# Optimization experiments

Measured on AMD Instinct MI355X. Metric: run time of the kernel, lower is better.

## Reference

```python
import jax, jax.numpy as jnp
import numpy as np

D_MODEL = 1024
N_HEADS = 16
HEAD_DIM = D_MODEL // N_HEADS
BATCH = 2
SEQ = 2048


def setup_inputs() -> dict:
    key = jax.random.key(0)
    ks = jax.random.split(key, 9)
    s = 1.0 / np.sqrt(D_MODEL)
    inp = {
        "x": jax.random.normal(ks[0], (BATCH, SEQ, D_MODEL), dtype=jnp.float32),
        "Wq": jax.random.uniform(ks[1], (D_MODEL, D_MODEL), jnp.float32, -s, s),
        "bq": jax.random.uniform(ks[2], (D_MODEL,), jnp.float32, -s, s),
        "Wk": jax.random.uniform(ks[3], (D_MODEL, D_MODEL), jnp.float32, -s, s),
        "bk": jax.random.uniform(ks[4], (D_MODEL,), jnp.float32, -s, s),
        "Wv": jax.random.uniform(ks[5], (D_MODEL, D_MODEL), jnp.float32, -s, s),
        "bv": jax.random.uniform(ks[6], (D_MODEL,), jnp.float32, -s, s),
        "Wo": jax.random.uniform(ks[7], (D_MODEL, D_MODEL), jnp.float32, -s, s),
        "bo": jax.random.uniform(ks[8], (D_MODEL,), jnp.float32, -s, s),
    }
    return inp


def reference(x, Wq, bq, Wk, bk, Wv, bv, Wo, bo):
    B, S, _ = x.shape
    # projections -> [B, H, S, Dh]
    def proj(W, b):
        y = jnp.einsum('bsd,df->bsf', x, W) + b
        return y.reshape(B, S, N_HEADS, HEAD_DIM).transpose(0, 2, 1, 3)
    q = proj(Wq, bq)
    k = proj(Wk, bk)
    v = proj(Wv, bv)
    scores = jnp.einsum('bhqd,bhkd->bhqk', q, k) / jnp.sqrt(jnp.float32(HEAD_DIM))
    mask = jnp.tril(jnp.ones((S, S), dtype=bool))  # [S, S] causal mask
    scores = jnp.where(mask, scores, -jnp.inf)
    weights = jax.nn.softmax(scores, axis=-1)
    h = jnp.einsum('bhqk,bhkd->bhqd', weights, v)
    h = h.transpose(0, 2, 1, 3).reshape(B, S, N_HEADS * HEAD_DIM)
    return jnp.einsum('bsd,df->bsf', h, Wo) + bo
```

## Files before the change

kernel.cpp:

```cpp
#include <hip/hip_runtime.h>
#include <hip/hip_bf16.h>
#include <cmath>

#define D_MODEL 1024
#define NHEADS 16
#define HDIM 64
#define BATCH 2
#define SEQ 2048
#define MROWS (BATCH*SEQ)
#define KDIM 1024

typedef unsigned short ushort_t;
typedef unsigned int uint32;
typedef __attribute__((ext_vector_type(8))) short short8;
typedef __attribute__((ext_vector_type(4))) float floatx4;

#define QSCALE 0.1803368801111204f
#define EXP2F(x) __builtin_amdgcn_exp2f(x)

__device__ __forceinline__ ushort_t f2bf(float x) {
    union { float f; uint32 u; } v; v.f = x;
    uint32 r = v.u + 0x7FFFu + ((v.u >> 16) & 1u);
    return (ushort_t)(r >> 16);
}

__device__ __forceinline__ uint32 pkbf(float a, float b) {
    union { __hip_bfloat162 h2; uint32 u; } v;
    v.h2 = __float22bfloat162_rn(make_float2(a, b));
    return v.u;
}

__device__ __forceinline__ void glds16(const void* g, void* l) {
    __builtin_amdgcn_global_load_lds(
        (const __attribute__((address_space(1))) void*)g,
        (__attribute__((address_space(3))) void*)l, 16, 0, 0);
}

__global__ __launch_bounds__(256)
void cvt_all(const float* __restrict__ x, const float* __restrict__ W0,
             const float* __restrict__ W1, const float* __restrict__ W2,
             const float* __restrict__ W3, ushort_t* __restrict__ xb,
             ushort_t* __restrict__ WtQKV, ushort_t* __restrict__ WtO)
{
    const int z = blockIdx.z;
    if (z == 4) {
        size_t idx = ((size_t)blockIdx.y * 32 + blockIdx.x) * 256 + threadIdx.x;
        #pragma unroll
        for (int l = 0; l < 4; ++l) {
            size_t i = ((size_t)l * 262144 + idx) * 4;
            float4 v = *(const float4*)(x + i);
            uint2 o;
            o.x = pkbf(v.x, v.y);
            o.y = pkbf(v.z, v.w);
            *(uint2*)(xb + i) = o;
        }
        return;
    }
    __shared__ float tl[32][33];
    const float* W = (z == 0) ? W0 : (z == 1) ? W1 : (z == 2) ? W2 : W3;
    ushort_t* out = (z < 3) ? (WtQKV + (size_t)z * D_MODEL * KDIM) : WtO;
    const int k0 = blockIdx.x * 32, n0 = blockIdx.y * 32;
    const int tx = threadIdx.x & 31, ty = threadIdx.x >> 5;
    #pragma unroll
    for (int i = 0; i < 4; ++i)
        tl[ty + i * 8][tx] = W[(size_t)(k0 + ty + i * 8) * D_MODEL + n0 + tx];
    __syncthreads();
    #pragma unroll
    for (int i = 0; i < 4; ++i)
        out[(size_t)(n0 + ty + i * 8) * KDIM + k0 + tx] = f2bf(tl[tx][ty + i * 8]);
}

__global__ __launch_bounds__(128, 2)
void gemm_qkv(const ushort_t* __restrict__ A, const ushort_t* __restrict__ Bt,
              const float* __restrict__ b0, const float* __restrict__ b1,
              const float* __restrict__ b2, ushort_t* __restrict__ Qb,
              ushort_t* __restrict__ Kb, ushort_t* __restrict__ Vb)
{
    __shared__ ushort_t As[128 * 64];
    __shared__ ushort_t Bs[128 * 64];

    const int tid = threadIdx.x;
    const int w = tid >> 6, lane = tid & 63;
    const int quad = lane >> 4, col = lane & 15;
    const int m0 = blockIdx.y * 128, n0 = blockIdx.x * 128;

    floatx4 zero = {0.f, 0.f, 0.f, 0.f};
    floatx4 acc[4][8];
    #pragma unroll
    for (int i = 0; i < 4; ++i)
        #pragma unroll
        for (int j = 0; j < 8; ++j) acc[i][j] = zero;

    #pragma unroll 1
    for (int k0 = 0; k0 < KDIM; k0 += 64) {
        #pragma unroll
        for (int i = 0; i < 8; ++i) {
            int c = i * 128 + tid;
            int row = c >> 3;
            int kc = (c & 7) ^ (row & 7);
            glds16(A  + (size_t)(m0 + row) * KDIM + k0 + kc * 8, As + (i * 128 + w * 64) * 8);
            glds16(Bt + (size_t)(n0 + row) * KDIM + k0 + kc * 8, Bs + (i * 128 + w * 64) * 8);
        }
        __syncthreads();
        #pragma unroll
        for (int ks = 0; ks < 2; ++ks) {
            short8 af[4], bfr[8];
            const int kc = ks * 4 + quad;
            #pragma unroll
            for (int mt = 0; mt < 4; ++mt) {
                int r = w * 64 + mt * 16 + col;
                af[mt] = *(const short8*)(As + ((size_t)r * 8 + (kc ^ (r & 7))) * 8);
            }
            #pragma unroll
            for (int nt = 0; nt < 8; ++nt) {
                int r = nt * 16 + col;
                bfr[nt] = *(const short8*)(Bs + ((size_t)r * 8 + (kc ^ (r & 7))) * 8);
            }
            #pragma unroll
            for (int mt = 0; mt < 4; ++mt)
                #pragma unroll
                for (int nt = 0; nt < 8; ++nt)
                    acc[mt][nt] = __builtin_amdgcn_mfma_f32_16x16x32_bf16(
                        af[mt], bfr[nt], acc[mt][nt], 0, 0, 0);
        }
        __syncthreads();
    }

    const int which = n0 >> 10;
    const float* bp = (which == 0) ? b0 : (which == 1) ? b1 : b2;
    if (which < 2) {
        ushort_t* outp = (which == 0) ? Qb : Kb;
        const float scl = (which == 0) ? QSCALE : 1.0f;
        #pragma unroll
        for (int mt = 0; mt < 4; ++mt)
            #pragma unroll
            for (int nt = 0; nt < 8; ++nt) {
                int nn = (n0 + nt * 16 + col) & 1023;
                float bb = bp[nn];
                int h = nn >> 6, d = nn & 63;
                #pragma unroll
                for (int r = 0; r < 4; ++r) {
                    int m = m0 + w * 64 + mt * 16 + quad * 4 + r;
                    int b = m >> 11, s = m & 2047;
                    outp[((size_t)(b * NHEADS + h) * SEQ + s) * HDIM + d] =
                        f2bf((acc[mt][nt][r] + bb) * scl);
                }
            }
    } else {
        #pragma unroll
        for (int mt = 0; mt < 4; ++mt)
            #pragma unroll
            for (int nt = 0; nt < 8; ++nt) {
                int nn = (n0 + nt * 16 + col) & 1023;
                float bb = bp[nn];
                int h = nn >> 6, d = nn & 63;
                int mb = m0 + w * 64 + mt * 16 + quad * 4;
                int b = mb >> 11, s = mb & 2047;
                uint2 pw;
                pw.x = pkbf(acc[mt][nt][0] + bb, acc[mt][nt][1] + bb);
                pw.y = pkbf(acc[mt][nt][2] + bb, acc[mt][nt][3] + bb);
                *(uint2*)(Vb + ((size_t)(b * NHEADS + h) * HDIM + d) * SEQ + s) = pw;
            }
    }
}

__global__ __launch_bounds__(128, 2)
void gemm_o(const ushort_t* __restrict__ A, const ushort_t* __restrict__ Bt,
            const float* __restrict__ b0, float* __restrict__ Cf)
{
    __shared__ ushort_t As[128 * 64];
    __shared__ ushort_t Bs[64 * 64];

    const int tid = threadIdx.x;
    const int w = tid >> 6, lane = tid & 63;
    const int quad = lane >> 4, col = lane & 15;
    const int m0 = blockIdx.y * 128, n0 = blockIdx.x * 64;

    floatx4 zero = {0.f, 0.f, 0.f, 0.f};
    floatx4 acc[4][4];
    #pragma unroll
    for (int i = 0; i < 4; ++i)
        #pragma unroll
        for (int j = 0; j < 4; ++j) acc[i][j] = zero;

    #pragma unroll 1
    for (int k0 = 0; k0 < KDIM; k0 += 64) {
        #pragma unroll
        for (int i = 0; i < 8; ++i) {
            int c = i * 128 + tid;
            int row = c >> 3;
            int kc = (c & 7) ^ (row & 7);
            glds16(A + (size_t)(m0 + row) * KDIM + k0 + kc * 8, As + (i * 128 + w * 64) * 8);
        }
        #pragma unroll
        for (int i = 0; i < 4; ++i) {
            int c = i * 128 + tid;
            int row = c >> 3;
            int kc = (c & 7) ^ (row & 7);
            glds16(Bt + (size_t)(n0 + row) * KDIM + k0 + kc * 8, Bs + (i * 128 + w * 64) * 8);
        }
        __syncthreads();
        #pragma unroll
        for (int ks = 0; ks < 2; ++ks) {
            short8 af[4], bfr[4];
            const int kc = ks * 4 + quad;
            #pragma unroll
            for (int mt = 0; mt < 4; ++mt) {
                int r = w * 64 + mt * 16 + col;
                af[mt] = *(const short8*)(As + ((size_t)r * 8 + (kc ^ (r & 7))) * 8);
            }
            #pragma unroll
            for (int nt = 0; nt < 4; ++nt) {
                int r = nt * 16 + col;
                bfr[nt] = *(const short8*)(Bs + ((size_t)r * 8 + (kc ^ (r & 7))) * 8);
            }
            #pragma unroll
            for (int mt = 0; mt < 4; ++mt)
                #pragma unroll
                for (int nt = 0; nt < 4; ++nt)
                    acc[mt][nt] = __builtin_amdgcn_mfma_f32_16x16x32_bf16(
                        af[mt], bfr[nt], acc[mt][nt], 0, 0, 0);
        }
        __syncthreads();
    }

    #pragma unroll
    for (int mt = 0; mt < 4; ++mt)
        #pragma unroll
        for (int nt = 0; nt < 4; ++nt) {
            int n = n0 + nt * 16 + col;
            float bb = b0[n];
            #pragma unroll
            for (int r = 0; r < 4; ++r) {
                int m = m0 + w * 64 + mt * 16 + quad * 4 + r;
                Cf[(size_t)m * D_MODEL + n] = acc[mt][nt][r] + bb;
            }
        }
}

__global__ __launch_bounds__(256)
void attn_mfma(const ushort_t* __restrict__ Q, const ushort_t* __restrict__ K,
               const ushort_t* __restrict__ Vt, ushort_t* __restrict__ H)
{
    __shared__ ushort_t Qs[64 * 64];
    __shared__ ushort_t Ks[2][64 * 64];
    __shared__ ushort_t Vs[2][64 * 64];
    ushort_t* Ps = Qs;

    const int tid = threadIdx.x;
    const int w = tid >> 6, lane = tid & 63;
    const int quad = lane >> 4, col = lane & 15;
    const int blk = blockIdx.x;
    const int bh = (blk & 7) * 4 + ((blk >> 3) & 3);
    const int pair = blk >> 5;
    const size_t base = (size_t)bh * SEQ * HDIM;
    const ushort_t* Kb = K + base;
    const ushort_t* Vb = Vt + base;
    const int b = bh >> 4, h = bh & 15;

    const int c0 = (w * 2 + 0) * 64 + lane;
    const int c1 = (w * 2 + 1) * 64 + lane;
    const int r0 = c0 >> 3, o0 = ((c0 & 7) ^ (r0 & 7)) * 8;
    const int r1 = c1 >> 3, o1 = ((c1 & 7) ^ (r1 & 7)) * 8;

    const int qloc = w * 16 + col;
    const int rq = qloc;
    const floatx4 zero = {0.f, 0.f, 0.f, 0.f};

    #pragma unroll 1
    for (int pi = 0; pi < 2; ++pi) {
        const int qt = pi ? pair : 31 - pair;
        const int q0 = qt * 64;
        const int nt = qt + 1;

        __syncthreads();
        #pragma unroll
        for (int i = 0; i < 2; ++i) {
            int c = (w * 2 + i) * 64 + lane;
            int row = c >> 3, kc = (c & 7) ^ (row & 7);
            glds16(Q + base + (size_t)(q0 + row) * HDIM + kc * 8, Qs + (w * 2 + i) * 512);
        }
        glds16(Kb + (size_t)r0 * HDIM + o0, Ks[0] + (w * 2 + 0) * 512);
        glds16(Kb + (size_t)r1 * HDIM + o1, Ks[0] + (w * 2 + 1) * 512);
        glds16(Vb + (size_t)r0 * SEQ + o0,  Vs[0] + (w * 2 + 0) * 512);
        glds16(Vb + (size_t)r1 * SEQ + o1,  Vs[0] + (w * 2 + 1) * 512);
        __syncthreads();

        short8 bq[2];
        #pragma unroll
        for (int ks = 0; ks < 2; ++ks) {
            int kc = ks * 4 + quad;
            bq[ks] = *(const short8*)(Qs + ((size_t)rq * 8 + (kc ^ (rq & 7))) * 8);
        }

        floatx4 o[4];
        #pragma unroll
        for (int j = 0; j < 4; ++j) o[j] = zero;
        float lreg = 0.f;

        #pragma unroll 1
        for (int t = 0; t < nt; ++t) {
            const ushort_t* Kcur = Ks[t & 1];
            const ushort_t* Vcur = Vs[t & 1];
            if (t + 1 < nt) {
                const int k0n = (t + 1) * 64;
                ushort_t* Kn = Ks[(t + 1) & 1];
                ushort_t* Vn = Vs[(t + 1) & 1];
                glds16(Kb + (size_t)(k0n + r0) * HDIM + o0, Kn + (w * 2 + 0) * 512);
                glds16(Kb + (size_t)(k0n + r1) * HDIM + o1, Kn + (w * 2 + 1) * 512);
                glds16(Vb + (size_t)r0 * SEQ + k0n + o0,    Vn + (w * 2 + 0) * 512);
                glds16(Vb + (size_t)r1 * SEQ + k0n + o1,    Vn + (w * 2 + 1) * 512);
            }

            floatx4 sc[4];
            #pragma unroll
            for (int j = 0; j < 4; ++j) sc[j] = zero;
            #pragma unroll
            for (int ks = 0; ks < 2; ++ks) {
                const int kc = ks * 4 + quad;
                #pragma unroll
                for (int j = 0; j < 4; ++j) {
                    int rk = j * 16 + col;
                    short8 ak = *(const short8*)(Kcur + ((size_t)rk * 8 + (kc ^ (rk & 7))) * 8);
                    sc[j] = __builtin_amdgcn_mfma_f32_16x16x32_bf16(ak, bq[ks], sc[j], 0, 0, 0);
                }
            }

            if (t == nt - 1) {
                #pragma unroll
                for (int j = 0; j < 4; ++j)
                    #pragma unroll
                    for (int r = 0; r < 4; ++r)
                        if (j * 16 + quad * 4 + r > qloc) sc[j][r] = -INFINITY;
            }

            float ls = 0.f;
            #pragma unroll
            for (int j = 0; j < 4; ++j) {
                float p0 = EXP2F(sc[j][0]);
                float p1 = EXP2F(sc[j][1]);
                float p2 = EXP2F(sc[j][2]);
                float p3 = EXP2F(sc[j][3]);
                ls += (p0 + p1) + (p2 + p3);
                uint2 pw;
                pw.x = pkbf(p0, p1);
                pw.y = pkbf(p2, p3);
                int c = 2 * j + (quad >> 1);
                *(uint2*)(Ps + ((size_t)rq * 8 + (c ^ (rq & 7))) * 8 + (quad & 1) * 4) = pw;
            }
            lreg += ls;

            #pragma unroll
            for (int ks = 0; ks < 2; ++ks) {
                const int kc = ks * 4 + quad;
                short8 bp = *(const short8*)(Ps + ((size_t)rq * 8 + (kc ^ (rq & 7))) * 8);
                #pragma unroll
                for (int j = 0; j < 4; ++j) {
                    int rv = j * 16 + col;
                    short8 av = *(const short8*)(Vcur + ((size_t)rv * 8 + (kc ^ (rv & 7))) * 8);
                    o[j] = __builtin_amdgcn_mfma_f32_16x16x32_bf16(av, bp, o[j], 0, 0, 0);
                }
            }

            __syncthreads();
        }

        lreg += __shfl_xor(lreg, 16);
        lreg += __shfl_xor(lreg, 32);

        const float linv = 1.f / lreg;
        const size_t rowb = ((size_t)(b * SEQ + q0 + qloc)) * D_MODEL + h * HDIM;
        #pragma unroll
        for (int j = 0; j < 4; ++j) {
            uint2 pw;
            pw.x = pkbf(o[j][0] * linv, o[j][1] * linv);
            pw.y = pkbf(o[j][2] * linv, o[j][3] * linv);
            *(uint2*)(H + rowb + j * 16 + quad * 4) = pw;
        }
    }
}

extern "C" void kernel_launch(void* const* d_in, const int* in_sizes, int n_in,
                              void* d_out, int out_size, void* d_ws, size_t ws_size,
                              hipStream_t stream)
{
    (void)in_sizes; (void)n_in; (void)out_size; (void)ws_size;
    const float* x  = (const float*)d_in[0];
    const float* Wq = (const float*)d_in[1];
    const float* bq = (const float*)d_in[2];
    const float* Wk = (const float*)d_in[3];
    const float* bk = (const float*)d_in[4];
    const float* Wv = (const float*)d_in[5];
    const float* bv = (const float*)d_in[6];
    const float* Wo = (const float*)d_in[7];
    const float* bo = (const float*)d_in[8];

    const size_t E = (size_t)MROWS * D_MODEL;
    ushort_t* xb    = (ushort_t*)d_ws;
    ushort_t* WtQKV = xb + E;
    ushort_t* WtO   = WtQKV + 3 * (size_t)D_MODEL * KDIM;
    ushort_t* Qb    = WtO + (size_t)D_MODEL * KDIM;
    ushort_t* Kb    = Qb + E;
    ushort_t* Vb    = Kb + E;
    ushort_t* Hb    = Vb + E;

    cvt_all<<<dim3(32, 32, 5), 256, 0, stream>>>(x, Wq, Wk, Wv, Wo, xb, WtQKV, WtO);
    gemm_qkv<<<dim3(24, 32), 128, 0, stream>>>(xb, WtQKV, bq, bk, bv, Qb, Kb, Vb);
    attn_mfma<<<dim3(512), 256, 0, stream>>>(Qb, Kb, Vb, Hb);
    gemm_o<<<dim3(16, 32), 128, 0, stream>>>(Hb, WtO, bo, (float*)d_out);
}
```

Before: 179.0 us.

## Split attention key tile across waves and reduce partial outputs in shared memory

Each wave now owns 16 keys of the 64-key tile and computes scores for all 64 queries, instead of owning 16 queries against all keys. This removes the P round-trip through shared memory, since P stays in registers and feeds 16x16x16 MFMAs directly. Partial O and row sums are reduced across the four waves through a 66KB shared buffer at the end. In exchange it uses more accumulator registers (64 floats for O), more LDS (which may lower occupancy), and adds a cross-wave reduction on each query tile.

```diff
diff --git a/kernel.cpp b/kernel.cpp
--- a/kernel.cpp
+++ b/kernel.cpp
@@ -13,6 +13,7 @@
 typedef unsigned short ushort_t;
 typedef unsigned int uint32;
 typedef __attribute__((ext_vector_type(8))) short short8;
+typedef __attribute__((ext_vector_type(4))) short short4b;
 typedef __attribute__((ext_vector_type(4))) float floatx4;
 
 #define QSCALE 0.1803368801111204f
@@ -242,10 +243,12 @@
 void attn_mfma(const ushort_t* __restrict__ Q, const ushort_t* __restrict__ K,
                const ushort_t* __restrict__ Vt, ushort_t* __restrict__ H)
 {
-    __shared__ ushort_t Qs[64 * 64];
-    __shared__ ushort_t Ks[2][64 * 64];
-    __shared__ ushort_t Vs[2][64 * 64];
-    ushort_t* Ps = Qs;
+    __shared__ __align__(16) float smemf[16640];
+    ushort_t* Qs  = (ushort_t*)smemf;
+    ushort_t* Ksm = (ushort_t*)(smemf + 2048);
+    ushort_t* Vsm = (ushort_t*)(smemf + 6144);
+    float* Ored = smemf;
+    float* Lred = smemf + 16384;
 
     const int tid = threadIdx.x;
     const int w = tid >> 6, lane = tid & 63;
@@ -263,8 +266,7 @@
     const int r0 = c0 >> 3, o0 = ((c0 & 7) ^ (r0 & 7)) * 8;
     const int r1 = c1 >> 3, o1 = ((c1 & 7) ^ (r1 & 7)) * 8;
 
-    const int qloc = w * 16 + col;
-    const int rq = qloc;
+    const int rk = w * 16 + col;
     const floatx4 zero = {0.f, 0.f, 0.f, 0.f};
 
     #pragma unroll 1
@@ -280,32 +282,37 @@
             int row = c >> 3, kc = (c & 7) ^ (row & 7);
             glds16(Q + base + (size_t)(q0 + row) * HDIM + kc * 8, Qs + (w * 2 + i) * 512);
         }
-        glds16(Kb + (size_t)r0 * HDIM + o0, Ks[0] + (w * 2 + 0) * 512);
-        glds16(Kb + (size_t)r1 * HDIM + o1, Ks[0] + (w * 2 + 1) * 512);
-        glds16(Vb + (size_t)r0 * SEQ + o0,  Vs[0] + (w * 2 + 0) * 512);
-        glds16(Vb + (size_t)r1 * SEQ + o1,  Vs[0] + (w * 2 + 1) * 512);
-        __syncthreads();
-
-        short8 bq[2];
-        #pragma unroll
-        for (int ks = 0; ks < 2; ++ks) {
-            int kc = ks * 4 + quad;
-            bq[ks] = *(const short8*)(Qs + ((size_t)rq * 8 + (kc ^ (rq & 7))) * 8);
-        }
-
-        floatx4 o[4];
-        #pragma unroll
-        for (int j = 0; j < 4; ++j) o[j] = zero;
-        float lreg = 0.f;
+        glds16(Kb + (size_t)r0 * HDIM + o0, Ksm + (w * 2 + 0) * 512);
+        glds16(Kb + (size_t)r1 * HDIM + o1, Ksm + (w * 2 + 1) * 512);
+        glds16(Vb + (size_t)r0 * SEQ + o0,  Vsm + (w * 2 + 0) * 512);
+        glds16(Vb + (size_t)r1 * SEQ + o1,  Vsm + (w * 2 + 1) * 512);
+        __syncthreads();
+
+        short8 bq[4][2];
+        #pragma unroll
+        for (int qb = 0; qb < 4; ++qb)
+            #pragma unroll
+            for (int ks = 0; ks < 2; ++ks) {
+                int rq = qb * 16 + col;
+                int kc = ks * 4 + quad;
+                bq[qb][ks] = *(const short8*)(Qs + ((size_t)rq * 8 + (kc ^ (rq & 7))) * 8);
+            }
+
+        floatx4 o_[4][4];
+        #pragma unroll
+        for (int i = 0; i < 4; ++i)
+            #pragma unroll
+            for (int j = 0; j < 4; ++j) o_[i][j] = zero;
+        float lq[4] = {0.f, 0.f, 0.f, 0.f};
 
         #pragma unroll 1
         for (int t = 0; t < nt; ++t) {
-            const ushort_t* Kcur = Ks[t & 1];
-            const ushort_t* Vcur = Vs[t & 1];
+            const ushort_t* Kcur = Ksm + (t & 1) * 4096;
+            const ushort_t* Vcur = Vsm + (t & 1) * 4096;
             if (t + 1 < nt) {
                 const int k0n = (t + 1) * 64;
-                ushort_t* Kn = Ks[(t + 1) & 1];
-                ushort_t* Vn = Vs[(t + 1) & 1];
+                ushort_t* Kn = Ksm + ((t + 1) & 1) * 4096;
+                ushort_t* Vn = Vsm + ((t + 1) & 1) * 4096;
                 glds16(Kb + (size_t)(k0n + r0) * HDIM + o0, Kn + (w * 2 + 0) * 512);
                 glds16(Kb + (size_t)(k0n + r1) * HDIM + o1, Kn + (w * 2 + 1) * 512);
                 glds16(Vb + (size_t)r0 * SEQ + k0n + o0,    Vn + (w * 2 + 0) * 512);
@@ -314,68 +321,104 @@
 
             floatx4 sc[4];
             #pragma unroll
-            for (int j = 0; j < 4; ++j) sc[j] = zero;
+            for (int qb = 0; qb < 4; ++qb) sc[qb] = zero;
             #pragma unroll
             for (int ks = 0; ks < 2; ++ks) {
                 const int kc = ks * 4 + quad;
-                #pragma unroll
-                for (int j = 0; j < 4; ++j) {
-                    int rk = j * 16 + col;
-                    short8 ak = *(const short8*)(Kcur + ((size_t)rk * 8 + (kc ^ (rk & 7))) * 8);
-                    sc[j] = __builtin_amdgcn_mfma_f32_16x16x32_bf16(ak, bq[ks], sc[j], 0, 0, 0);
-                }
+                short8 ak = *(const short8*)(Kcur + ((size_t)rk * 8 + (kc ^ (rk & 7))) * 8);
+                #pragma unroll
+                for (int qb = 0; qb < 4; ++qb)
+                    sc[qb] = __builtin_amdgcn_mfma_f32_16x16x32_bf16(
+                        ak, bq[qb][ks], sc[qb], 0, 0, 0);
             }
 
             if (t == nt - 1) {
                 #pragma unroll
-                for (int j = 0; j < 4; ++j)
+                for (int qb = 0; qb < 4; ++qb)
                     #pragma unroll
                     for (int r = 0; r < 4; ++r)
-                        if (j * 16 + quad * 4 + r > qloc) sc[j][r] = -INFINITY;
-            }
-
-            float ls = 0.f;
+                        if (w * 16 + quad * 4 + r > qb * 16 + col) sc[qb][r] = -INFINITY;
+            }
+
+            short4b bp[4];
+            #pragma unroll
+            for (int qb = 0; qb < 4; ++qb) {
+                float p0 = EXP2F(sc[qb][0]);
+                float p1 = EXP2F(sc[qb][1]);
+                float p2 = EXP2F(sc[qb][2]);
+                float p3 = EXP2F(sc[qb][3]);
+                lq[qb] += (p0 + p1) + (p2 + p3);
+                union { uint2 u; short4b s; } pv;
+                pv.u.x = pkbf(p0, p1);
+                pv.u.y = pkbf(p2, p3);
+                bp[qb] = pv.s;
+            }
+
+            const int cc = 2 * w + (quad >> 1);
+            const int sub = (quad & 1) * 4;
+            #pragma unroll
+            for (int db = 0; db < 4; ++db) {
+                int rv = db * 16 + col;
+                short4b av = *(const short4b*)(Vcur + ((size_t)rv * 8 + (cc ^ (rv & 7))) * 8 + sub);
+                #pragma unroll
+                for (int qb = 0; qb < 4; ++qb)
+                    o_[db][qb] = __builtin_amdgcn_mfma_f32_16x16x16bf16_1k(
+                        av, bp[qb], o_[db][qb], 0, 0, 0);
+            }
+
+            __syncthreads();
+        }
+
+        #pragma unroll
+        for (int qb = 0; qb < 4; ++qb) {
+            lq[qb] += __shfl_xor(lq[qb], 16);
+            lq[qb] += __shfl_xor(lq[qb], 32);
+        }
+        if (quad == 0) {
+            #pragma unroll
+            for (int qb = 0; qb < 4; ++qb) Lred[w * 64 + qb * 16 + col] = lq[qb];
+        }
+        {
+            float* myreg = Ored + w * 4096;
+            #pragma unroll
+            for (int db = 0; db < 4; ++db)
+                #pragma unroll
+                for (int qb = 0; qb < 4; ++qb) {
+                    int q = qb * 16 + col;
+                    int swch = (db * 4 + quad) ^ col;
+                    *(floatx4*)(myreg + q * 64 + swch * 4) = o_[db][qb];
+                }
+        }
+        __syncthreads();
+
+        {
+            const int qloc = w * 16 + (lane >> 2);
+            float lsum = Lred[qloc] + Lred[64 + qloc] + Lred[128 + qloc] + Lred[192 + qloc];
+            float linv = 1.f / lsum;
+            const int dc0 = (lane & 3) * 4;
+            floatx4 acc[4];
             #pragma unroll
             for (int j = 0; j < 4; ++j) {
-                float p0 = EXP2F(sc[j][0]);
-                float p1 = EXP2F(sc[j][1]);
-                float p2 = EXP2F(sc[j][2]);
-                float p3 = EXP2F(sc[j][3]);
-                ls += (p0 + p1) + (p2 + p3);
-                uint2 pw;
-                pw.x = pkbf(p0, p1);
-                pw.y = pkbf(p2, p3);
-                int c = 2 * j + (quad >> 1);
-                *(uint2*)(Ps + ((size_t)rq * 8 + (c ^ (rq & 7))) * 8 + (quad & 1) * 4) = pw;
-            }
-            lreg += ls;
-
-            #pragma unroll
-            for (int ks = 0; ks < 2; ++ks) {
-                const int kc = ks * 4 + quad;
-                short8 bp = *(const short8*)(Ps + ((size_t)rq * 8 + (kc ^ (rq & 7))) * 8);
-                #pragma unroll
-                for (int j = 0; j < 4; ++j) {
-                    int rv = j * 16 + col;
-                    short8 av = *(const short8*)(Vcur + ((size_t)rv * 8 + (kc ^ (rv & 7))) * 8);
-                    o[j] = __builtin_amdgcn_mfma_f32_16x16x32_bf16(av, bp, o[j], 0, 0, 0);
-                }
-            }
-
-            __syncthreads();
-        }
-
-        lreg += __shfl_xor(lreg, 16);
-        lreg += __shfl_xor(lreg, 32);
-
-        const float linv = 1.f / lreg;
-        const size_t rowb = ((size_t)(b * SEQ + q0 + qloc)) * D_MODEL + h * HDIM;
-        #pragma unroll
-        for (int j = 0; j < 4; ++j) {
-            uint2 pw;
-            pw.x = pkbf(o[j][0] * linv, o[j][1] * linv);
-            pw.y = pkbf(o[j][2] * linv, o[j][3] * linv);
-            *(uint2*)(H + rowb + j * 16 + quad * 4) = pw;
+                int swch = (dc0 + j) ^ (qloc & 15);
+                const float* p = Ored + (size_t)qloc * 64 + swch * 4;
+                floatx4 a = *(const floatx4*)p;
+                a += *(const floatx4*)(p + 4096);
+                a += *(const floatx4*)(p + 8192);
+                a += *(const floatx4*)(p + 12288);
+                acc[j] = a;
+            }
+            const size_t rowb = ((size_t)(b * SEQ + q0 + qloc)) * D_MODEL + h * HDIM + dc0 * 4;
+            uint4 u0, u1;
+            u0.x = pkbf(acc[0][0] * linv, acc[0][1] * linv);
+            u0.y = pkbf(acc[0][2] * linv, acc[0][3] * linv);
+            u0.z = pkbf(acc[1][0] * linv, acc[1][1] * linv);
+            u0.w = pkbf(acc[1][2] * linv, acc[1][3] * linv);
+            u1.x = pkbf(acc[2][0] * linv, acc[2][1] * linv);
+            u1.y = pkbf(acc[2][2] * linv, acc[2][3] * linv);
+            u1.z = pkbf(acc[3][0] * linv, acc[3][1] * linv);
+            u1.w = pkbf(acc[3][2] * linv, acc[3][3] * linv);
+            *(uint4*)(H + rowb) = u0;
+            *(uint4*)(H + rowb + 8) = u1;
         }
     }
 }
```

Result: no change. 179.2 us (+0.1%).
